# Kernel optimization log

Measured on AMD Instinct MI355X. Metric: run time of the kernel, lower is better.

The kernel has to match this reference:

```python
import jax, jax.numpy as jnp
import numpy as np

ENT_N = 100000  # entity vocab (relation rows live inside this table, as in the source)
REL_N = 237
DIM = 128
N = 16384       # batch of triples
EPS = 1e-12     # F.normalize default eps


def _l2norm(x, axis=-1):
    n = jnp.linalg.norm(x, axis=axis, keepdims=True)
    return x / jnp.maximum(n, EPS)


def setup_inputs() -> dict:
    key = jax.random.key(0)
    k1, k2, k3, k4 = jax.random.split(key, 4)
    ent_emb = jax.random.normal(k1, (ENT_N, DIM), dtype=jnp.float32)
    h_ids = jax.random.randint(k2, (N,), 0, ENT_N)
    r_typ = jax.random.randint(k3, (N,), 0, REL_N)
    t_ids = jax.random.randint(k4, (N,), 0, ENT_N)
    return {"ent_emb": ent_emb, "h_ids": h_ids, "r_typ": r_typ, "t_ids": t_ids}


def reference(ent_emb, h_ids, r_typ, t_ids):
    d = ent_emb.shape[1]
    h = _l2norm(ent_emb[h_ids])           # [n, d]
    t = _l2norm(ent_emb[t_ids])           # [n, d]
    # The torch loop looks up ent_emb[r_typ*d + k] for k in range(d); gather
    # the whole relation block at once instead of d tiny lookups + cat.
    r_idx = r_typ[:, None] * d + jnp.arange(d)  # [n, d]
    R = ent_emb[r_idx]                     # [n, d, d]; row k = relation vec k
    prod = jnp.einsum('nd,nkd->nk', h, R)  # [n, d]
    prod = _l2norm(prod)
    return jnp.linalg.norm(prod - t, axis=1)  # [n]
```

## Files before the change

### kernel.cpp

```cpp
#include <hip/hip_runtime.h>

#define RELS 237
#define DIM 128
#define CH 32
#define MAXCHUNK 742
#define PREPB 64
#define EPS 1e-12f

typedef __attribute__((ext_vector_type(8))) short bf16x8;
typedef __attribute__((ext_vector_type(4))) float f32x4;


__device__ __forceinline__ unsigned short f2bf(float f) {
    unsigned int u = __float_as_uint(f);
    u = (u + 0x7fffu + ((u >> 16) & 1u)) >> 16;
    return (unsigned short)u;
}

__global__ __launch_bounds__(256) void k_prep(const int* __restrict__ r_typ,
                                              const int* __restrict__ h_ids,
                                              const int* __restrict__ t_ids,
                                              int* __restrict__ ws, int n) {
    __shared__ int hist[256];
    __shared__ int offs[256];
    __shared__ int scn[256];
    const int t = threadIdx.x;
    hist[t] = 0;
    __syncthreads();

    for (int i = blockIdx.x * 256 + t; i < n; i += PREPB * 256)
        atomicAdd(&hist[r_typ[i]], 1);
    __syncthreads();
    if (t < RELS && hist[t] > 0) atomicAdd(&ws[t], hist[t]);

    __syncthreads();
    __threadfence();
    if (t == 0) {
        atomicAdd(&ws[254], 1);
        while (atomicAdd(&ws[254], 0) < PREPB) __builtin_amdgcn_s_sleep(2);
    }
    __syncthreads();
    __threadfence();

    const int c = (t < RELS) ? atomicAdd(&ws[t], 0) : 0;
    scn[t] = c; __syncthreads();
    #pragma unroll
    for (int off = 1; off < 256; off <<= 1) {
        int v = (t >= off) ? scn[t - off] : 0;
        __syncthreads();
        scn[t] += v; __syncthreads();
    }
    offs[t] = scn[t] - c;
    __syncthreads();

    if (blockIdx.x == 0) {
        const int nch = (c + CH - 1) >> 5;
        scn[t] = nch; __syncthreads();
        #pragma unroll
        for (int off = 1; off < 256; off <<= 1) {
            int v = (t >= off) ? scn[t - off] : 0;
            __syncthreads();
            scn[t] += v; __syncthreads();
        }
        const int choff = scn[t] - nch;
        if (t == 255) ws[1000] = scn[255];
        for (int j = 0; j < nch; ++j) {
            int cb  = offs[t] + j * CH;
            int len = c - j * CH; if (len > CH) len = CH;
            ws[1024 + choff + j] = (t << 20) | (cb << 6) | len;
        }
    }

    for (int i = blockIdx.x * 256 + t; i < n; i += PREPB * 256) {
        int rr  = r_typ[i];
        int hi  = h_ids[i];
        int ti  = t_ids[i];
        int pos = offs[rr] + atomicAdd(&ws[512 + rr], 1);
        ws[2048  + pos] = i;
        ws[18432 + pos] = hi;
        ws[34816 + pos] = ti;
    }
}

__global__ __launch_bounds__(256, 3) void relgemm(
    const float* __restrict__ ent,
    const int*   __restrict__ ws,
    float*       __restrict__ out)
{
    __shared__ char smem[43776];
    unsigned short* Rb = (unsigned short*)smem;
    unsigned short* Hb = (unsigned short*)(smem + 34816);
    int*  sidx = (int*)(smem + 43520);
    int*  tRow = (int*)(smem + 43648);
    float* Pp  = (float*)smem;

    const int cid = blockIdx.x;
    if (cid >= ws[1000]) return;
    const int e    = ws[1024 + cid];
    const int r    = e >> 20;
    const int base = (e >> 6) & 16383;
    const int len  = e & 63;
    const int* sortedIdx = ws + 2048;
    const int* shid      = ws + 18432;
    const int* stid      = ws + 34816;

    const int tid  = threadIdx.x;
    const int lane = tid & 63;
    const int w    = tid >> 6;

    if (tid < CH) {
        int tc = tid < len ? tid : len - 1;
        sidx[tid] = sortedIdx[base + tc];
        tRow[tid] = stid[base + tc];
    }

    #pragma unroll
    for (int s = 0; s < 4; ++s) {
        int g = s * 256 + tid;
        int trow = g >> 5, c4 = g & 31;
        int tc = trow < len ? trow : len - 1;
        int hid = shid[base + tc];
        float4 v = ((const float4*)ent)[((long)hid << 5) + c4];
        ushort4 b; b.x = f2bf(v.x); b.y = f2bf(v.y); b.z = f2bf(v.z); b.w = f2bf(v.w);
        *(ushort4*)(Hb + trow * 136 + c4 * 4) = b;
    }
    const float4* Rg = (const float4*)ent + ((long)r << 12);
    #pragma unroll
    for (int s = 0; s < 16; ++s) {
        int g = s * 256 + tid;
        int row = g >> 5, c4 = g & 31;
        float4 v = Rg[g];
        ushort4 b; b.x = f2bf(v.x); b.y = f2bf(v.y); b.z = f2bf(v.z); b.w = f2bf(v.w);
        *(ushort4*)(Rb + row * 136 + c4 * 4) = b;
    }
    __syncthreads();

    const int q = lane >> 4, c = lane & 15;
    const unsigned short* A0p = Hb + c * 136 + q * 8;
    const unsigned short* A1p = Hb + (c + 16) * 136 + q * 8;
    const unsigned short* B0p = Rb + (w * 32 + c) * 136 + q * 8;
    const unsigned short* B1p = Rb + (w * 32 + 16 + c) * 136 + q * 8;

    f32x4 a00 = {0.f,0.f,0.f,0.f}, a01 = a00, a10 = a00, a11 = a00;
    #pragma unroll
    for (int ks = 0; ks < 4; ++ks) {
        bf16x8 A0 = *(const bf16x8*)(A0p + ks * 32);
        bf16x8 A1 = *(const bf16x8*)(A1p + ks * 32);
        bf16x8 B0 = *(const bf16x8*)(B0p + ks * 32);
        bf16x8 B1 = *(const bf16x8*)(B1p + ks * 32);
        a00 = __builtin_amdgcn_mfma_f32_16x16x32_bf16(A0, B0, a00, 0, 0, 0);
        a01 = __builtin_amdgcn_mfma_f32_16x16x32_bf16(A0, B1, a01, 0, 0, 0);
        a10 = __builtin_amdgcn_mfma_f32_16x16x32_bf16(A1, B0, a10, 0, 0, 0);
        a11 = __builtin_amdgcn_mfma_f32_16x16x32_bf16(A1, B1, a11, 0, 0, 0);
    }
    __syncthreads();

    #pragma unroll
    for (int reg = 0; reg < 4; ++reg) {
        int m0 = q * 4 + reg;
        Pp[m0 * 132        + w * 32      + c] = a00[reg];
        Pp[m0 * 132        + w * 32 + 16 + c] = a01[reg];
        Pp[(m0 + 16) * 132 + w * 32      + c] = a10[reg];
        Pp[(m0 + 16) * 132 + w * 32 + 16 + c] = a11[reg];
    }
    __syncthreads();

    float p0v[8], p1v[8], t0v[8], t1v[8];
    #pragma unroll
    for (int tt = 0; tt < 8; ++tt) {
        int t = w * 8 + tt;
        int trow = tRow[t];
        const float* tv = ent + ((long)trow << 7);
        t0v[tt] = tv[lane];
        t1v[tt] = tv[lane + 64];
        p0v[tt] = Pp[t * 132 + lane];
        p1v[tt] = Pp[t * 132 + 64 + lane];
    }
    #pragma unroll
    for (int tt = 0; tt < 8; ++tt) {
        int t   = w * 8 + tt;
        float p0 = p0v[tt], p1 = p1v[tt];
        float tv0 = t0v[tt], tv1 = t1v[tt];
        float sp  = p0 * p0 + p1 * p1;
        float st  = tv0 * tv0 + tv1 * tv1;
        float spt = p0 * tv0 + p1 * tv1;
        #pragma unroll
        for (int m = 32; m >= 1; m >>= 1) {
            sp  += __shfl_xor(sp,  m, 64);
            st  += __shfl_xor(st,  m, 64);
            spt += __shfl_xor(spt, m, 64);
        }
        if (lane == 0 && t < len) {
            float npn = fmaxf(sqrtf(sp), EPS);
            float ntn = fmaxf(sqrtf(st), EPS);
            float v   = 2.0f - 2.0f * (spt / (npn * ntn));
            out[sidx[t]] = sqrtf(fmaxf(v, 0.0f));
        }
    }
}

extern "C" void kernel_launch(void* const* d_in, const int* in_sizes, int n_in,
                              void* d_out, int out_size, void* d_ws, size_t ws_size,
                              hipStream_t stream) {
    const float* ent   = (const float*)d_in[0];
    const int*   h_ids = (const int*)d_in[1];
    const int*   r_typ = (const int*)d_in[2];
    const int*   t_ids = (const int*)d_in[3];
    float* out = (float*)d_out;
    int*   ws  = (int*)d_ws;
    const int n = in_sizes[1];

    hipMemsetAsync(ws, 0, 4096, stream);
    hipLaunchKernelGGL(k_prep,  dim3(PREPB),    dim3(256), 0, stream,
                       r_typ, h_ids, t_ids, ws, n);
    hipLaunchKernelGGL(relgemm, dim3(MAXCHUNK), dim3(256), 0, stream,
                       ent, ws, out);
}
```

Baseline: 119.3 us.

## Pre-convert relation blocks to MFMA-ordered bf16 and read B directly from global

Adds a k_conv kernel that converts each relation's 128x128 block to bf16 once per call, in the exact fragment order the MFMA B operand needs. relgemm then loads B fragments straight from this global buffer instead of converting a relation block into LDS in every chunk. That shrinks LDS use from about 43 KB to 17 KB and raises launch bounds occupancy from 3 to 4 blocks. The cost is an extra kernel launch, a full pass over 237 relation blocks, and uncoalesced-risk global B loads that now sit on the MFMA critical path.

```diff
diff --git a/kernel.cpp b/kernel.cpp
--- a/kernel.cpp
+++ b/kernel.cpp
@@ -15,6 +15,30 @@
     unsigned int u = __float_as_uint(f);
     u = (u + 0x7fffu + ((u >> 16) & 1u)) >> 16;
     return (unsigned short)u;
+}
+
+__global__ __launch_bounds__(256) void k_conv(const float* __restrict__ ent,
+                                              unsigned short* __restrict__ Rc) {
+    const int r = blockIdx.x, tid = threadIdx.x;
+    const float* src = ent + ((long)r << 14);
+    unsigned short* dst = Rc + ((long)r << 14);
+    #pragma unroll
+    for (int s = 0; s < 8; ++s) {
+        int idx = s * 256 + tid;
+        int c  = idx & 15;
+        int q  = (idx >> 4) & 3;
+        int ks = (idx >> 6) & 3;
+        int nt = idx >> 8;
+        const float* sp = src + (nt * 16 + c) * 128 + ks * 32 + q * 8;
+        float4 v0 = *(const float4*)sp;
+        float4 v1 = *(const float4*)(sp + 4);
+        uint4 wv;
+        wv.x = f2bf(v0.x) | ((unsigned)f2bf(v0.y) << 16);
+        wv.y = f2bf(v0.z) | ((unsigned)f2bf(v0.w) << 16);
+        wv.z = f2bf(v1.x) | ((unsigned)f2bf(v1.y) << 16);
+        wv.w = f2bf(v1.z) | ((unsigned)f2bf(v1.w) << 16);
+        *(uint4*)(dst + (long)idx * 8) = wv;
+    }
 }
 
 __global__ __launch_bounds__(256) void k_prep(const int* __restrict__ r_typ,
@@ -82,17 +106,17 @@
     }
 }
 
-__global__ __launch_bounds__(256, 3) void relgemm(
-    const float* __restrict__ ent,
-    const int*   __restrict__ ws,
-    float*       __restrict__ out)
+__global__ __launch_bounds__(256, 4) void relgemm(
+    const float*          __restrict__ ent,
+    const unsigned short* __restrict__ Rc,
+    const int*            __restrict__ ws,
+    float*                __restrict__ out)
 {
-    __shared__ char smem[43776];
-    unsigned short* Rb = (unsigned short*)smem;
-    unsigned short* Hb = (unsigned short*)(smem + 34816);
-    int*  sidx = (int*)(smem + 43520);
-    int*  tRow = (int*)(smem + 43648);
+    __shared__ char smem[17152];
+    unsigned short* Hb = (unsigned short*)smem;
     float* Pp  = (float*)smem;
+    int*  sidx = (int*)(smem + 16896);
+    int*  tRow = (int*)(smem + 17024);
 
     const int cid = blockIdx.x;
     if (cid >= ws[1000]) return;
@@ -100,9 +124,6 @@
     const int r    = e >> 20;
     const int base = (e >> 6) & 16383;
     const int len  = e & 63;
-    const int* sortedIdx = ws + 2048;
-    const int* shid      = ws + 18432;
-    const int* stid      = ws + 34816;
 
     const int tid  = threadIdx.x;
     const int lane = tid & 63;
@@ -110,8 +131,8 @@
 
     if (tid < CH) {
         int tc = tid < len ? tid : len - 1;
-        sidx[tid] = sortedIdx[base + tc];
-        tRow[tid] = stid[base + tc];
+        sidx[tid] = ws[2048  + base + tc];
+        tRow[tid] = ws[34816 + base + tc];
     }
 
     #pragma unroll
@@ -119,35 +140,25 @@
         int g = s * 256 + tid;
         int trow = g >> 5, c4 = g & 31;
         int tc = trow < len ? trow : len - 1;
-        int hid = shid[base + tc];
+        int hid = ws[18432 + base + tc];
         float4 v = ((const float4*)ent)[((long)hid << 5) + c4];
         ushort4 b; b.x = f2bf(v.x); b.y = f2bf(v.y); b.z = f2bf(v.z); b.w = f2bf(v.w);
         *(ushort4*)(Hb + trow * 136 + c4 * 4) = b;
     }
-    const float4* Rg = (const float4*)ent + ((long)r << 12);
-    #pragma unroll
-    for (int s = 0; s < 16; ++s) {
-        int g = s * 256 + tid;
-        int row = g >> 5, c4 = g & 31;
-        float4 v = Rg[g];
-        ushort4 b; b.x = f2bf(v.x); b.y = f2bf(v.y); b.z = f2bf(v.z); b.w = f2bf(v.w);
-        *(ushort4*)(Rb + row * 136 + c4 * 4) = b;
-    }
     __syncthreads();
 
     const int q = lane >> 4, c = lane & 15;
     const unsigned short* A0p = Hb + c * 136 + q * 8;
     const unsigned short* A1p = Hb + (c + 16) * 136 + q * 8;
-    const unsigned short* B0p = Rb + (w * 32 + c) * 136 + q * 8;
-    const unsigned short* B1p = Rb + (w * 32 + 16 + c) * 136 + q * 8;
+    const unsigned short* Bp  = Rc + ((long)r << 14) + w * 4096 + q * 128 + c * 8;
 
     f32x4 a00 = {0.f,0.f,0.f,0.f}, a01 = a00, a10 = a00, a11 = a00;
     #pragma unroll
     for (int ks = 0; ks < 4; ++ks) {
+        bf16x8 B0 = *(const bf16x8*)(Bp + ks * 512);
+        bf16x8 B1 = *(const bf16x8*)(Bp + 2048 + ks * 512);
         bf16x8 A0 = *(const bf16x8*)(A0p + ks * 32);
         bf16x8 A1 = *(const bf16x8*)(A1p + ks * 32);
-        bf16x8 B0 = *(const bf16x8*)(B0p + ks * 32);
-        bf16x8 B1 = *(const bf16x8*)(B1p + ks * 32);
         a00 = __builtin_amdgcn_mfma_f32_16x16x32_bf16(A0, B0, a00, 0, 0, 0);
         a01 = __builtin_amdgcn_mfma_f32_16x16x32_bf16(A0, B1, a01, 0, 0, 0);
         a10 = __builtin_amdgcn_mfma_f32_16x16x32_bf16(A1, B0, a10, 0, 0, 0);
@@ -208,11 +219,13 @@
     const int*   t_ids = (const int*)d_in[3];
     float* out = (float*)d_out;
     int*   ws  = (int*)d_ws;
+    unsigned short* Rc = (unsigned short*)(ws + 65536);
     const int n = in_sizes[1];
 
     hipMemsetAsync(ws, 0, 4096, stream);
+    hipLaunchKernelGGL(k_conv,  dim3(RELS),     dim3(256), 0, stream, ent, Rc);
     hipLaunchKernelGGL(k_prep,  dim3(PREPB),    dim3(256), 0, stream,
                        r_typ, h_ids, t_ids, ws, n);
     hipLaunchKernelGGL(relgemm, dim3(MAXCHUNK), dim3(256), 0, stream,
-                       ent, ws, out);
-}
+                       ent, Rc, ws, out);
+}
```

After: 121.0 us. No clear change (+1.5%).
